# Performance work log

Hardware: AMD Instinct MI355X
Metric: run time of the kernel (lower is better)

Reference implementation:

```python
import jax, jax.numpy as jnp
import numpy as np

N_TOKENS = 8192      # codebook size K
HIDDEN = 256         # hidden_size H
N = 8192             # batch of latent vectors (vmapped dim)
COMMITMENT_COST = 0.25


def setup_inputs() -> dict:
    key = jax.random.key(0)
    k_h, k_cb, _ = jax.random.split(key, 3)
    h = jax.random.normal(k_h, (N, HIDDEN), dtype=jnp.float32)
    # codebook initialized exactly as in __init__: normal * 0.1
    codebook = jax.random.normal(k_cb, (N_TOKENS, HIDDEN), dtype=jnp.float32) * 0.1
    temperature = jnp.ones((), dtype=jnp.float32)  # unused, API compat
    return {"h": h, "temperature": temperature, "codebook": codebook}


def reference(h, temperature, codebook):
    """Batched VQ quantization: one-hot nearest-codebook weights + commitment loss.

    h: (N, H) float32, codebook: (K, H) float32. Returns (hard (N,K), loss (N,)).
    """
    del temperature  # VQ is always hard; kept for API compatibility
    K = codebook.shape[0]
    # squared distances ||h - c||^2 = ||h||^2 - 2 h.c + ||c||^2, avoids (N,K,H) tensor
    h_sq = jnp.sum(h * h, axis=-1, keepdims=True)              # (N, 1)
    c_sq = jnp.sum(codebook * codebook, axis=-1)               # (K,)
    dists = h_sq - 2.0 * jnp.einsum('nh,kh->nk', h, codebook) + c_sq[None, :]  # (N, K)
    idx = jnp.argmin(dists, axis=-1)                           # (N,)
    hard = jax.nn.one_hot(idx, K, dtype=h.dtype)               # (N, K)
    # STE wrapping from __call__ (gradient of hard is zero anyway)
    hard = jax.lax.stop_gradient(hard)
    # commitment_loss (per token), matching the module's method
    z_q = codebook[idx]                                        # (N, H) gather
    codebook_loss = jnp.mean((jax.lax.stop_gradient(h) - z_q) ** 2, axis=-1)
    commit_loss = jnp.mean((h - jax.lax.stop_gradient(z_q)) ** 2, axis=-1)
    loss = codebook_loss + COMMITMENT_COST * commit_loss       # (N,)
    return hard, loss
```

## Files before the change

kernel.cpp:

```cpp
#include <hip/hip_runtime.h>
#include <hip/hip_bf16.h>
#include <math.h>

#define N_ROWS   8192
#define K_CODES  8192
#define H_DIM    256
#define NSPLIT   8
#define KSPLIT   (K_CODES / NSPLIT)
#define MARGIN   5e-4f

typedef short short8 __attribute__((ext_vector_type(8)));
typedef float f32x4  __attribute__((ext_vector_type(4)));

#define C2_OFF      0
#define H2_OFF      8192
#define BESTP_OFF   16384
#define SECONDP_OFF (BESTP_OFF + 8*8192)
#define IDXP_OFF    (SECONDP_OFF + 8*8192)
#define DISTF_OFF   (IDXP_OFF + 8*8192)
#define IDXF_OFF    (DISTF_OFF + 8192)
#define GAP_OFF     (IDXF_OFF + 8192)
#define FCNT_OFF    245760
#define FLIST_OFF   245776
#define PBEST_OFF   245840
#define PIDX_OFF    (PBEST_OFF + 8192)
#define MAXSLOT     64

#define PK_AHI ((size_t)0)
#define PK_ALO ((size_t)4 << 20)
#define PK_BHI ((size_t)8 << 20)
#define PK_BLO ((size_t)12 << 20)

__device__ __forceinline__ void async_copy16(const void* g, void* l) {
    __builtin_amdgcn_global_load_lds(
        (const __attribute__((address_space(1))) unsigned int*)g,
        (__attribute__((address_space(3))) unsigned int*)l, 16, 0, 0);
}

__device__ __forceinline__ void conv2(float a, float b, unsigned& hi, unsigned& lo) {
    float2 p0 = make_float2(a, b);
    __hip_bfloat162 hb = __float22bfloat162_rn(p0);
    unsigned h = *(unsigned*)&hb;
    hi = h;
    float ra = a - __uint_as_float(h << 16);
    float rb = b - __uint_as_float(h & 0xFFFF0000u);
    float2 p1 = make_float2(ra, rb);
    __hip_bfloat162 lb = __float22bfloat162_rn(p1);
    lo = *(unsigned*)&lb;
}

__global__ __launch_bounds__(256) void prep_sq(const float* __restrict__ h,
                                               const float* __restrict__ cb,
                                               float* __restrict__ ws) {
    if (blockIdx.x == 0 && threadIdx.x == 0) ((int*)ws)[FCNT_OFF] = 0;
    int blk  = blockIdx.x;
    int wave = threadIdx.x >> 6;
    int lane = threadIdx.x & 63;
    bool isH = blk >= 2048;
    int idx  = (isH ? (blk - 2048) : blk) * 4 + wave;
    const float* src = isH ? h : cb;
    const float4* p = (const float4*)(src + (size_t)idx * H_DIM);
    float4 v = p[lane];
    float s = v.x*v.x + v.y*v.y + v.z*v.z + v.w*v.w;
    #pragma unroll
    for (int off = 32; off > 0; off >>= 1) s += __shfl_down(s, off, 64);
    if (lane == 0) ws[(isH ? H2_OFF : C2_OFF) + idx] = s;
}

__global__ __launch_bounds__(256) void pack_kernel(const float* __restrict__ h,
                                                   const float* __restrict__ cb,
                                                   char* __restrict__ out) {
    int w    = threadIdx.x >> 6;
    int lane = threadIdx.x & 63;
    int ln15 = lane & 15;
    int kg   = lane >> 4;
    bool isB = blockIdx.x >= 1024;
    int u = ((blockIdx.x & 1023) << 2) + w;
    int p = u >> 3, c = u & 7;
    const float* src = isB ? cb : h;
    char* hiB = out + (isB ? PK_BHI : PK_AHI);
    char* loB = out + (isB ? PK_BLO : PK_ALO);
    const float* s = src + (size_t)(p * 16 + ln15) * H_DIM + c * 32 + kg * 8;
    float4 v0 = *(const float4*)s;
    float4 v1 = *(const float4*)(s + 4);
    unsigned h0, h1, h2, h3, l0, l1, l2, l3;
    conv2(v0.x, v0.y, h0, l0);
    conv2(v0.z, v0.w, h1, l1);
    conv2(v1.x, v1.y, h2, l2);
    conv2(v1.z, v1.w, h3, l3);
    size_t off = ((size_t)u * 64 + lane) * 16;
    *(uint4*)(hiB + off) = make_uint4(h0, h1, h2, h3);
    *(uint4*)(loB + off) = make_uint4(l0, l1, l2, l3);
}

__global__ __launch_bounds__(256, 2) void vq_min_kernel(const char* __restrict__ pk,
                                                        float* __restrict__ ws) {
    __shared__ __align__(16) char smem[35840];
    const int tid  = threadIdx.x;
    const int w    = tid >> 6;
    const int lane = tid & 63;
    const int ln15 = lane & 15;
    const int kg   = lane >> 4;
    const int wm   = (w >> 1) * 64;
    const int wn   = (w & 1) * 64;
    const int am   = (w >> 1) * 4;
    const int bn4  = (w & 1) * 4;

    const int rowpan0 = blockIdx.x * 8;
    const int bpan0   = blockIdx.y * 64;
    const float* c2g = ws + C2_OFF;

    const size_t pkoff = (w == 0) ? PK_AHI : (w == 1) ? PK_ALO : (w == 2) ? PK_BHI : PK_BLO;
    char* lwave = smem + w * 8192;

    float best16[16], sec16[16];
    int   idx16[16];
    #pragma unroll
    for (int t = 0; t < 16; t++) { best16[t] = 3.4e38f; sec16[t] = 3.4e38f; idx16[t] = 0; }

    #pragma unroll 1
    for (int ct = 0; ct < 8; ++ct) {
        const int kb   = blockIdx.y * KSPLIT + ct * 128;
        const int pan0 = (w < 2) ? rowpan0 : (bpan0 + ct * 8);
        f32x4 acc[4][4];
        #pragma unroll
        for (int i = 0; i < 4; i++)
            #pragma unroll
            for (int j = 0; j < 4; j++) acc[i][j] = (f32x4){0.f, 0.f, 0.f, 0.f};

        #pragma unroll 1
        for (int kc = 0; kc < 8; ++kc) {
            __syncthreads();
            #pragma unroll
            for (int q = 0; q < 8; ++q) {
                const char* g = pk + pkoff + (((size_t)(pan0 + q) * 8 + kc) * 64 + lane) * 16;
                async_copy16(g, lwave + q * 1024);
            }
            __syncthreads();

            short8 ah[4], al[4], bh[4], bl[4];
            #pragma unroll
            for (int i = 0; i < 4; i++) {
                int o = ((am + i) * 64 + lane) * 16;
                ah[i] = *(const short8*)(smem + o);
                al[i] = *(const short8*)(smem + 8192 + o);
            }
            #pragma unroll
            for (int j = 0; j < 4; j++) {
                int o = ((bn4 + j) * 64 + lane) * 16;
                bh[j] = *(const short8*)(smem + 16384 + o);
                bl[j] = *(const short8*)(smem + 24576 + o);
            }
            #pragma unroll
            for (int i = 0; i < 4; i++)
                #pragma unroll
                for (int j = 0; j < 4; j++) {
                    acc[i][j] = __builtin_amdgcn_mfma_f32_16x16x32_bf16(ah[i], bh[j], acc[i][j], 0, 0, 0);
                    acc[i][j] = __builtin_amdgcn_mfma_f32_16x16x32_bf16(al[i], bh[j], acc[i][j], 0, 0, 0);
                    acc[i][j] = __builtin_amdgcn_mfma_f32_16x16x32_bf16(ah[i], bl[j], acc[i][j], 0, 0, 0);
                }
        }

        float cv[4];
        #pragma unroll
        for (int j = 0; j < 4; j++) cv[j] = c2g[kb + wn + j * 16 + ln15];
        #pragma unroll
        for (int i = 0; i < 4; i++)
            #pragma unroll
            for (int reg = 0; reg < 4; reg++) {
                const int t = i * 4 + reg;
                #pragma unroll
                for (int j = 0; j < 4; j++) {
                    float d = cv[j] - 2.f * acc[i][j][reg];
                    int   k = kb + wn + j * 16 + ln15;
                    if (d < best16[t])      { sec16[t] = best16[t]; best16[t] = d; idx16[t] = k; }
                    else if (d < sec16[t])  { sec16[t] = d; }
                }
            }
    }

    #pragma unroll
    for (int t = 0; t < 16; t++) {
        float b = best16[t], s2 = sec16[t];
        int   bi = idx16[t];
        #pragma unroll
        for (int m = 1; m <= 8; m <<= 1) {
            float ob = __shfl_xor(b, m, 64);
            float os = __shfl_xor(s2, m, 64);
            int   oi = __shfl_xor(bi, m, 64);
            if (ob < b)      { s2 = fminf(b, os); b = ob; bi = oi; }
            else if (ob > b) { s2 = fminf(s2, ob); }
            else             { if (oi < bi) bi = oi; s2 = b; }
        }
        best16[t] = b; sec16[t] = s2; idx16[t] = bi;
    }
    float* mb = (float*)(smem + 32768);
    float* ms = (float*)(smem + 32768 + 1024);
    int*   mi = (int*)(smem + 32768 + 2048);
    if (ln15 == 0) {
        #pragma unroll
        for (int i = 0; i < 4; i++)
            #pragma unroll
            for (int reg = 0; reg < 4; reg++) {
                int r = wm + i * 16 + kg * 4 + reg;
                int half = (w & 1);
                mb[r * 2 + half] = best16[i * 4 + reg];
                ms[r * 2 + half] = sec16[i * 4 + reg];
                mi[r * 2 + half] = idx16[i * 4 + reg];
            }
    }
    __syncthreads();
    if (tid < 128) {
        float b  = mb[tid * 2],     s2 = ms[tid * 2];
        int   bi = mi[tid * 2];
        float ob = mb[tid * 2 + 1], os = ms[tid * 2 + 1];
        int   oi = mi[tid * 2 + 1];
        if (ob < b)      { s2 = fminf(b, os); b = ob; bi = oi; }
        else if (ob > b) { s2 = fminf(s2, ob); }
        else             { if (oi < bi) bi = oi; s2 = b; }
        int row = blockIdx.x * 128 + tid;
        int s   = blockIdx.y;
        ws[BESTP_OFF   + s * N_ROWS + row] = b;
        ws[SECONDP_OFF + s * N_ROWS + row] = s2;
        ((int*)ws)[IDXP_OFF + s * N_ROWS + row] = bi;
    }
}

__global__ __launch_bounds__(256) void merge_kernel(float* __restrict__ ws) {
    int row = blockIdx.x * blockDim.x + threadIdx.x;
    if (row >= N_ROWS) return;
    float b  = ws[BESTP_OFF + row];
    float s2 = ws[SECONDP_OFF + row];
    int   bi = ((int*)ws)[IDXP_OFF + row];
    for (int s = 1; s < NSPLIT; s++) {
        float ob = ws[BESTP_OFF   + s * N_ROWS + row];
        float os = ws[SECONDP_OFF + s * N_ROWS + row];
        int   oi = ((int*)ws)[IDXP_OFF + s * N_ROWS + row];
        if (ob < b)      { s2 = fminf(b, os); b = ob; bi = oi; }
        else if (ob > b) { s2 = fminf(s2, ob); }
        else             { if (oi < bi) bi = oi; s2 = b; }
    }
    float h2 = ws[H2_OFF + row];
    ws[DISTF_OFF + row] = h2 + b;
    ((int*)ws)[IDXF_OFF + row] = bi;
    if (s2 - b <= MARGIN) {
        int slot = atomicAdd(&((int*)ws)[FCNT_OFF], 1);
        if (slot < MAXSLOT) ((int*)ws)[FLIST_OFF + slot] = row;
    }
}

__global__ __launch_bounds__(256) void fixup_part(const float* __restrict__ h,
                                                  const float* __restrict__ cb,
                                                  float* __restrict__ ws) {
    int slot = blockIdx.y;
    int n = ((const int*)ws)[FCNT_OFF];
    if (n > MAXSLOT) n = MAXSLOT;
    if (slot >= n) return;
    int row   = ((const int*)ws)[FLIST_OFF + slot];
    int base  = blockIdx.x * 128;
    int wv    = threadIdx.x >> 6;
    int lane  = threadIdx.x & 63;
    float4 hv = *(const float4*)(h + (size_t)row * H_DIM + lane * 4);

    double best = 1e300;
    int    bi   = 1 << 30;
    for (int c = base + wv; c < base + 128; c += 4) {
        float4 cv = *(const float4*)(cb + (size_t)c * H_DIM + lane * 4);
        float dx = hv.x - cv.x, dy = hv.y - cv.y, dz = hv.z - cv.z, dw = hv.w - cv.w;
        double s = (double)dx * dx + (double)dy * dy + (double)dz * dz + (double)dw * dw;
        #pragma unroll
        for (int off = 32; off > 0; off >>= 1) s += __shfl_down(s, off, 64);
        if (lane == 0 && s < best) { best = s; bi = c; }
    }
    __shared__ double sb[4];
    __shared__ int    si[4];
    if (lane == 0) { sb[wv] = best; si[wv] = bi; }
    __syncthreads();
    if (threadIdx.x == 0) {
        double b = sb[0]; int x = si[0];
        for (int t = 1; t < 4; t++)
            if (sb[t] < b || (sb[t] == b && si[t] < x)) { b = sb[t]; x = si[t]; }
        ((double*)(ws + PBEST_OFF))[slot * 64 + blockIdx.x] = b;
        ((int*)ws)[PIDX_OFF + slot * 64 + blockIdx.x] = x;
    }
}

__global__ __launch_bounds__(64) void fixup_final(float* __restrict__ ws) {
    int slot = blockIdx.x;
    int n = ((const int*)ws)[FCNT_OFF];
    if (n > MAXSLOT) n = MAXSLOT;
    if (slot >= n) return;
    int lane = threadIdx.x;
    double b = ((const double*)(ws + PBEST_OFF))[slot * 64 + lane];
    int    x = ((const int*)ws)[PIDX_OFF + slot * 64 + lane];
    #pragma unroll
    for (int off = 32; off > 0; off >>= 1) {
        double ob = __shfl_down(b, off, 64);
        int    oi = __shfl_down(x, off, 64);
        if (ob < b || (ob == b && oi < x)) { b = ob; x = oi; }
    }
    if (lane == 0) {
        int row = ((const int*)ws)[FLIST_OFF + slot];
        ws[DISTF_OFF + row] = (float)b;
        ((int*)ws)[IDXF_OFF + row] = x;
    }
}

__global__ __launch_bounds__(256) void writeout_kernel(const float* __restrict__ ws,
                                                       float* __restrict__ out) {
    int row = blockIdx.x;
    int tid = threadIdx.x;
    int bi  = ((const int*)ws)[IDXF_OFF + row];
    float4* orow = (float4*)(out + (size_t)row * K_CODES);
    #pragma unroll
    for (int i = 0; i < 8; i++) {
        int f4 = tid + 256 * i;
        float4 v = make_float4(0.f, 0.f, 0.f, 0.f);
        if ((bi >> 2) == f4) ((float*)&v)[bi & 3] = 1.0f;
        orow[f4] = v;
    }
    if (tid == 0) {
        out[(size_t)N_ROWS * K_CODES + row] = (1.25f / 256.f) * ws[DISTF_OFF + row];
    }
}

extern "C" void kernel_launch(void* const* d_in, const int* in_sizes, int n_in,
                              void* d_out, int out_size, void* d_ws, size_t ws_size,
                              hipStream_t stream) {
    const float* h  = (const float*)d_in[0];
    const float* cb = (const float*)d_in[2];
    float* out = (float*)d_out;
    float* ws  = (float*)d_ws;

    prep_sq<<<4096, 256, 0, stream>>>(h, cb, ws);
    pack_kernel<<<2048, 256, 0, stream>>>(h, cb, (char*)d_out);
    vq_min_kernel<<<dim3(N_ROWS / 128, NSPLIT), 256, 0, stream>>>((const char*)d_out, ws);
    merge_kernel<<<N_ROWS / 256, 256, 0, stream>>>(ws);
    fixup_part<<<dim3(64, MAXSLOT), 256, 0, stream>>>(h, cb, ws);
    fixup_final<<<MAXSLOT, 64, 0, stream>>>(ws);
    writeout_kernel<<<N_ROWS, 256, 0, stream>>>(ws, out);
}
```

Measured before the change: 469.9 us.

## Widen codebook tile to 256 columns per block with shared LDS loads

Each block now processes 128 rows by 256 codebook columns per outer iteration instead of 128x128, halving the number of column tiles and reusing each A tile across twice as many MFMAs. LDS staging is redistributed so all waves cooperatively load 12 panels each, and the accumulator grows to 4x8 per wave. This raises LDS use to 48KB and register pressure, and the occupancy hint of 2 blocks per CU is dropped, which may lower occupancy. A barrier is added before reusing shared memory for the reduction scratch.

Result: slower. 612.9 us (+30.4%).

```diff
diff --git a/kernel.cpp b/kernel.cpp
--- a/kernel.cpp
+++ b/kernel.cpp
@@ -93,25 +93,21 @@
     *(uint4*)(loB + off) = make_uint4(l0, l1, l2, l3);
 }
 
-__global__ __launch_bounds__(256, 2) void vq_min_kernel(const char* __restrict__ pk,
-                                                        float* __restrict__ ws) {
-    __shared__ __align__(16) char smem[35840];
+__global__ __launch_bounds__(256) void vq_min_kernel(const char* __restrict__ pk,
+                                                     float* __restrict__ ws) {
+    __shared__ __align__(16) char smem[49152];
     const int tid  = threadIdx.x;
     const int w    = tid >> 6;
     const int lane = tid & 63;
     const int ln15 = lane & 15;
     const int kg   = lane >> 4;
     const int wm   = (w >> 1) * 64;
-    const int wn   = (w & 1) * 64;
+    const int wn   = (w & 1) * 128;
     const int am   = (w >> 1) * 4;
-    const int bn4  = (w & 1) * 4;
+    const int bn   = (w & 1) * 8;
 
     const int rowpan0 = blockIdx.x * 8;
-    const int bpan0   = blockIdx.y * 64;
     const float* c2g = ws + C2_OFF;
-
-    const size_t pkoff = (w == 0) ? PK_AHI : (w == 1) ? PK_ALO : (w == 2) ? PK_BHI : PK_BLO;
-    char* lwave = smem + w * 8192;
 
     float best16[16], sec16[16];
     int   idx16[16];
@@ -119,58 +115,66 @@
     for (int t = 0; t < 16; t++) { best16[t] = 3.4e38f; sec16[t] = 3.4e38f; idx16[t] = 0; }
 
     #pragma unroll 1
-    for (int ct = 0; ct < 8; ++ct) {
-        const int kb   = blockIdx.y * KSPLIT + ct * 128;
-        const int pan0 = (w < 2) ? rowpan0 : (bpan0 + ct * 8);
-        f32x4 acc[4][4];
+    for (int ct = 0; ct < 4; ++ct) {
+        const int kb      = blockIdx.y * KSPLIT + ct * 256;
+        const int colpan0 = kb >> 4;
+        f32x4 acc[4][8];
         #pragma unroll
         for (int i = 0; i < 4; i++)
             #pragma unroll
-            for (int j = 0; j < 4; j++) acc[i][j] = (f32x4){0.f, 0.f, 0.f, 0.f};
+            for (int j = 0; j < 8; j++) acc[i][j] = (f32x4){0.f, 0.f, 0.f, 0.f};
 
         #pragma unroll 1
         for (int kc = 0; kc < 8; ++kc) {
             __syncthreads();
             #pragma unroll
-            for (int q = 0; q < 8; ++q) {
-                const char* g = pk + pkoff + (((size_t)(pan0 + q) * 8 + kc) * 64 + lane) * 16;
-                async_copy16(g, lwave + q * 1024);
+            for (int q = 0; q < 12; ++q) {
+                int s = w * 12 + q;
+                const char* g;
+                if (s < 16) {
+                    int half = s >> 3, pan = s & 7;
+                    g = pk + (half ? PK_ALO : PK_AHI)
+                           + (((size_t)(rowpan0 + pan) * 8 + kc) * 64 + lane) * 16;
+                } else {
+                    int t2 = s - 16, half = t2 >> 4, pan = t2 & 15;
+                    g = pk + (half ? PK_BLO : PK_BHI)
+                           + (((size_t)(colpan0 + pan) * 8 + kc) * 64 + lane) * 16;
+                }
+                async_copy16(g, smem + s * 1024);
             }
             __syncthreads();
 
-            short8 ah[4], al[4], bh[4], bl[4];
+            short8 ah[4], al[4];
             #pragma unroll
             for (int i = 0; i < 4; i++) {
-                int o = ((am + i) * 64 + lane) * 16;
+                int o = (am + i) * 1024 + lane * 16;
                 ah[i] = *(const short8*)(smem + o);
                 al[i] = *(const short8*)(smem + 8192 + o);
             }
             #pragma unroll
-            for (int j = 0; j < 4; j++) {
-                int o = ((bn4 + j) * 64 + lane) * 16;
-                bh[j] = *(const short8*)(smem + 16384 + o);
-                bl[j] = *(const short8*)(smem + 24576 + o);
-            }
-            #pragma unroll
-            for (int i = 0; i < 4; i++)
+            for (int j = 0; j < 8; j++) {
+                int o = (bn + j) * 1024 + lane * 16;
+                short8 bh = *(const short8*)(smem + 16384 + o);
+                short8 bl = *(const short8*)(smem + 32768 + o);
                 #pragma unroll
-                for (int j = 0; j < 4; j++) {
-                    acc[i][j] = __builtin_amdgcn_mfma_f32_16x16x32_bf16(ah[i], bh[j], acc[i][j], 0, 0, 0);
-                    acc[i][j] = __builtin_amdgcn_mfma_f32_16x16x32_bf16(al[i], bh[j], acc[i][j], 0, 0, 0);
-                    acc[i][j] = __builtin_amdgcn_mfma_f32_16x16x32_bf16(ah[i], bl[j], acc[i][j], 0, 0, 0);
+                for (int i = 0; i < 4; i++) {
+                    acc[i][j] = __builtin_amdgcn_mfma_f32_16x16x32_bf16(ah[i], bh, acc[i][j], 0, 0, 0);
+                    acc[i][j] = __builtin_amdgcn_mfma_f32_16x16x32_bf16(al[i], bh, acc[i][j], 0, 0, 0);
+                    acc[i][j] = __builtin_amdgcn_mfma_f32_16x16x32_bf16(ah[i], bl, acc[i][j], 0, 0, 0);
                 }
+            }
         }
 
-        float cv[4];
-        #pragma unroll
-        for (int j = 0; j < 4; j++) cv[j] = c2g[kb + wn + j * 16 + ln15];
+        float cv[8];
+        #pragma unroll
+        for (int j = 0; j < 8; j++) cv[j] = c2g[kb + wn + j * 16 + ln15];
         #pragma unroll
         for (int i = 0; i < 4; i++)
             #pragma unroll
             for (int reg = 0; reg < 4; reg++) {
                 const int t = i * 4 + reg;
                 #pragma unroll
-                for (int j = 0; j < 4; j++) {
+                for (int j = 0; j < 8; j++) {
                     float d = cv[j] - 2.f * acc[i][j][reg];
                     int   k = kb + wn + j * 16 + ln15;
                     if (d < best16[t])      { sec16[t] = best16[t]; best16[t] = d; idx16[t] = k; }
@@ -194,9 +198,10 @@
         }
         best16[t] = b; sec16[t] = s2; idx16[t] = bi;
     }
-    float* mb = (float*)(smem + 32768);
-    float* ms = (float*)(smem + 32768 + 1024);
-    int*   mi = (int*)(smem + 32768 + 2048);
+    __syncthreads();
+    float* mb = (float*)smem;
+    float* ms = (float*)(smem + 1024);
+    int*   mi = (int*)(smem + 2048);
     if (ln15 == 0) {
         #pragma unroll
         for (int i = 0; i < 4; i++)
```

## Drop LDS staging in VQ distance kernel; per-wave direct global loads

Applied to the files above, without the earlier changes.

Rewrites the distance/argmin kernel so each wave independently handles a 64-row band by 512-code split and loads packed bf16 hi/lo fragments straight from global memory into registers. This removes the shared-memory staging, both __syncthreads per k-chunk and the cross-wave LDS reduction. NSPLIT rises to 16, and the partial best/second/index buffers move into the output buffer. The cost is the loss of intra-block operand sharing, so each wave re-reads A and B from L2/global, and latency hiding now depends on occupancy and unrolling.

Result: slower. 608.9 us (+29.6%).

```diff
diff --git a/kernel.cpp b/kernel.cpp
--- a/kernel.cpp
+++ b/kernel.cpp
@@ -5,8 +5,7 @@
 #define N_ROWS   8192
 #define K_CODES  8192
 #define H_DIM    256
-#define NSPLIT   8
-#define KSPLIT   (K_CODES / NSPLIT)
+#define NSPLIT   16
 #define MARGIN   5e-4f
 
 typedef short short8 __attribute__((ext_vector_type(8)));
@@ -14,15 +13,11 @@
 
 #define C2_OFF      0
 #define H2_OFF      8192
-#define BESTP_OFF   16384
-#define SECONDP_OFF (BESTP_OFF + 8*8192)
-#define IDXP_OFF    (SECONDP_OFF + 8*8192)
-#define DISTF_OFF   (IDXP_OFF + 8*8192)
+#define DISTF_OFF   16384
 #define IDXF_OFF    (DISTF_OFF + 8192)
-#define GAP_OFF     (IDXF_OFF + 8192)
-#define FCNT_OFF    245760
-#define FLIST_OFF   245776
-#define PBEST_OFF   245840
+#define FCNT_OFF    (IDXF_OFF + 8192)
+#define FLIST_OFF   (FCNT_OFF + 16)
+#define PBEST_OFF   (FLIST_OFF + 64)
 #define PIDX_OFF    (PBEST_OFF + 8192)
 #define MAXSLOT     64
 
@@ -30,12 +25,9 @@
 #define PK_ALO ((size_t)4 << 20)
 #define PK_BHI ((size_t)8 << 20)
 #define PK_BLO ((size_t)12 << 20)
-
-__device__ __forceinline__ void async_copy16(const void* g, void* l) {
-    __builtin_amdgcn_global_load_lds(
-        (const __attribute__((address_space(1))) unsigned int*)g,
-        (__attribute__((address_space(3))) unsigned int*)l, 16, 0, 0);
-}
+#define PART_BEST ((size_t)16 << 20)
+#define PART_SEC  (PART_BEST + (size_t)(NSPLIT * N_ROWS * 4))
+#define PART_IDX  (PART_SEC  + (size_t)(NSPLIT * N_ROWS * 4))
 
 __device__ __forceinline__ void conv2(float a, float b, unsigned& hi, unsigned& lo) {
     float2 p0 = make_float2(a, b);
@@ -93,25 +85,24 @@
     *(uint4*)(loB + off) = make_uint4(l0, l1, l2, l3);
 }
 
-__global__ __launch_bounds__(256, 2) void vq_min_kernel(const char* __restrict__ pk,
-                                                        float* __restrict__ ws) {
-    __shared__ __align__(16) char smem[35840];
-    const int tid  = threadIdx.x;
-    const int w    = tid >> 6;
-    const int lane = tid & 63;
-    const int ln15 = lane & 15;
-    const int kg   = lane >> 4;
-    const int wm   = (w >> 1) * 64;
-    const int wn   = (w & 1) * 64;
-    const int am   = (w >> 1) * 4;
-    const int bn4  = (w & 1) * 4;
-
-    const int rowpan0 = blockIdx.x * 8;
-    const int bpan0   = blockIdx.y * 64;
-    const float* c2g = ws + C2_OFF;
-
-    const size_t pkoff = (w == 0) ? PK_AHI : (w == 1) ? PK_ALO : (w == 2) ? PK_BHI : PK_BLO;
-    char* lwave = smem + w * 8192;
+__global__ __launch_bounds__(256, 1) void vq_min_kernel(const char* __restrict__ pk,
+                                                        const float* __restrict__ c2g,
+                                                        float* __restrict__ pbest,
+                                                        float* __restrict__ psec,
+                                                        int* __restrict__ pidx) {
+    const int w     = threadIdx.x >> 6;
+    const int lane  = threadIdx.x & 63;
+    const int ln15  = lane & 15;
+    const int kg    = lane >> 4;
+    const int g     = blockIdx.x * 4 + w;
+    const int band  = g >> 4;
+    const int split = g & 15;
+    const int lb    = lane * 16;
+
+    const char* Ah = pk + PK_AHI + (size_t)band * 32768 + lb;
+    const char* Al = pk + PK_ALO + (size_t)band * 32768 + lb;
+    const char* Bh = pk + PK_BHI + (size_t)split * (32 * 8192) + lb;
+    const char* Bl = pk + PK_BLO + (size_t)split * (32 * 8192) + lb;
 
     float best16[16], sec16[16];
     int   idx16[16];
@@ -120,36 +111,21 @@
 
     #pragma unroll 1
     for (int ct = 0; ct < 8; ++ct) {
-        const int kb   = blockIdx.y * KSPLIT + ct * 128;
-        const int pan0 = (w < 2) ? rowpan0 : (bpan0 + ct * 8);
         f32x4 acc[4][4];
         #pragma unroll
         for (int i = 0; i < 4; i++)
             #pragma unroll
             for (int j = 0; j < 4; j++) acc[i][j] = (f32x4){0.f, 0.f, 0.f, 0.f};
 
-        #pragma unroll 1
+        #pragma unroll 2
         for (int kc = 0; kc < 8; ++kc) {
-            __syncthreads();
-            #pragma unroll
-            for (int q = 0; q < 8; ++q) {
-                const char* g = pk + pkoff + (((size_t)(pan0 + q) * 8 + kc) * 64 + lane) * 16;
-                async_copy16(g, lwave + q * 1024);
-            }
-            __syncthreads();
-
             short8 ah[4], al[4], bh[4], bl[4];
             #pragma unroll
-            for (int i = 0; i < 4; i++) {
-                int o = ((am + i) * 64 + lane) * 16;
-                ah[i] = *(const short8*)(smem + o);
-                al[i] = *(const short8*)(smem + 8192 + o);
-            }
-            #pragma unroll
-            for (int j = 0; j < 4; j++) {
-                int o = ((bn4 + j) * 64 + lane) * 16;
-                bh[j] = *(const short8*)(smem + 16384 + o);
-                bl[j] = *(const short8*)(smem + 24576 + o);
+            for (int i = 0; i < 4; ++i) {
+                ah[i] = *(const short8*)(Ah + i * 8192 + kc * 1024);
+                al[i] = *(const short8*)(Al + i * 8192 + kc * 1024);
+                bh[i] = *(const short8*)(Bh + (size_t)(ct * 4 + i) * 8192 + kc * 1024);
+                bl[i] = *(const short8*)(Bl + (size_t)(ct * 4 + i) * 8192 + kc * 1024);
             }
             #pragma unroll
             for (int i = 0; i < 4; i++)
@@ -161,9 +137,10 @@
                 }
         }
 
+        const int kbase = split * 512 + ct * 64;
         float cv[4];
         #pragma unroll
-        for (int j = 0; j < 4; j++) cv[j] = c2g[kb + wn + j * 16 + ln15];
+        for (int j = 0; j < 4; j++) cv[j] = c2g[kbase + j * 16 + ln15];
         #pragma unroll
         for (int i = 0; i < 4; i++)
             #pragma unroll
@@ -172,7 +149,7 @@
                 #pragma unroll
                 for (int j = 0; j < 4; j++) {
                     float d = cv[j] - 2.f * acc[i][j][reg];
-                    int   k = kb + wn + j * 16 + ln15;
+                    int   k = kbase + j * 16 + ln15;
                     if (d < best16[t])      { sec16[t] = best16[t]; best16[t] = d; idx16[t] = k; }
                     else if (d < sec16[t])  { sec16[t] = d; }
                 }
@@ -194,48 +171,31 @@
         }
         best16[t] = b; sec16[t] = s2; idx16[t] = bi;
     }
-    float* mb = (float*)(smem + 32768);
-    float* ms = (float*)(smem + 32768 + 1024);
-    int*   mi = (int*)(smem + 32768 + 2048);
     if (ln15 == 0) {
         #pragma unroll
-        for (int i = 0; i < 4; i++)
-            #pragma unroll
-            for (int reg = 0; reg < 4; reg++) {
-                int r = wm + i * 16 + kg * 4 + reg;
-                int half = (w & 1);
-                mb[r * 2 + half] = best16[i * 4 + reg];
-                ms[r * 2 + half] = sec16[i * 4 + reg];
-                mi[r * 2 + half] = idx16[i * 4 + reg];
-            }
-    }
-    __syncthreads();
-    if (tid < 128) {
-        float b  = mb[tid * 2],     s2 = ms[tid * 2];
-        int   bi = mi[tid * 2];
-        float ob = mb[tid * 2 + 1], os = ms[tid * 2 + 1];
-        int   oi = mi[tid * 2 + 1];
-        if (ob < b)      { s2 = fminf(b, os); b = ob; bi = oi; }
-        else if (ob > b) { s2 = fminf(s2, ob); }
-        else             { if (oi < bi) bi = oi; s2 = b; }
-        int row = blockIdx.x * 128 + tid;
-        int s   = blockIdx.y;
-        ws[BESTP_OFF   + s * N_ROWS + row] = b;
-        ws[SECONDP_OFF + s * N_ROWS + row] = s2;
-        ((int*)ws)[IDXP_OFF + s * N_ROWS + row] = bi;
-    }
-}
-
-__global__ __launch_bounds__(256) void merge_kernel(float* __restrict__ ws) {
+        for (int t = 0; t < 16; t++) {
+            int i = t >> 2, reg = t & 3;
+            int row = band * 64 + i * 16 + kg * 4 + reg;
+            pbest[split * N_ROWS + row] = best16[t];
+            psec [split * N_ROWS + row] = sec16[t];
+            pidx [split * N_ROWS + row] = idx16[t];
+        }
+    }
+}
+
+__global__ __launch_bounds__(256) void merge_kernel(const float* __restrict__ pbest,
+                                                    const float* __restrict__ psec,
+                                                    const int* __restrict__ pidx,
+                                                    float* __restrict__ ws) {
     int row = blockIdx.x * blockDim.x + threadIdx.x;
     if (row >= N_ROWS) return;
-    float b  = ws[BESTP_OFF + row];
-    float s2 = ws[SECONDP_OFF + row];
-    int   bi = ((int*)ws)[IDXP_OFF + row];
+    float b  = pbest[row];
+    float s2 = psec[row];
+    int   bi = pidx[row];
     for (int s = 1; s < NSPLIT; s++) {
-        float ob = ws[BESTP_OFF   + s * N_ROWS + row];
-        float os = ws[SECONDP_OFF + s * N_ROWS + row];
-        int   oi = ((int*)ws)[IDXP_OFF + s * N_ROWS + row];
+        float ob = pbest[s * N_ROWS + row];
+        float os = psec [s * N_ROWS + row];
+        int   oi = pidx [s * N_ROWS + row];
         if (ob < b)      { s2 = fminf(b, os); b = ob; bi = oi; }
         else if (ob > b) { s2 = fminf(s2, ob); }
         else             { if (oi < bi) bi = oi; s2 = b; }
@@ -331,11 +291,16 @@
     const float* cb = (const float*)d_in[2];
     float* out = (float*)d_out;
     float* ws  = (float*)d_ws;
+    char*  pk  = (char*)d_out;
+
+    float* pbest = (float*)(pk + PART_BEST);
+    float* psec  = (float*)(pk + PART_SEC);
+    int*   pidx  = (int*)(pk + PART_IDX);
 
     prep_sq<<<4096, 256, 0, stream>>>(h, cb, ws);
-    pack_kernel<<<2048, 256, 0, stream>>>(h, cb, (char*)d_out);
-    vq_min_kernel<<<dim3(N_ROWS / 128, NSPLIT), 256, 0, stream>>>((const char*)d_out, ws);
-    merge_kernel<<<N_ROWS / 256, 256, 0, stream>>>(ws);
+    pack_kernel<<<2048, 256, 0, stream>>>(h, cb, pk);
+    vq_min_kernel<<<512, 256, 0, stream>>>(pk, ws, pbest, psec, pidx);
+    merge_kernel<<<N_ROWS / 256, 256, 0, stream>>>(pbest, psec, pidx, ws);
     fixup_part<<<dim3(64, MAXSLOT), 256, 0, stream>>>(h, cb, ws);
     fixup_final<<<MAXSLOT, 64, 0, stream>>>(ws);
     writeout_kernel<<<N_ROWS, 256, 0, stream>>>(ws, out);
```
